# Kernel tuning notes

Hardware: AMD Instinct MI355X
Metric: run time of the kernel (lower is better)

The kernel has to match this reference:

```python
import jax, jax.numpy as jnp
import numpy as np

D = 2048
N_PASSES = 2
TOKENS = 16384


def _wht_matrix(d):
    # Sylvester construction of the (unnormalized) Walsh-Hadamard matrix.
    h = np.array([[1.0]], dtype=np.float32)
    while h.shape[0] < d:
        h = np.block([[h, h], [h, -h]])
    return jnp.asarray(h)


def setup_inputs() -> dict:
    key = jax.random.key(0)
    kx, ks = jax.random.split(key)
    x = jax.random.normal(kx, (TOKENS, D), dtype=jnp.float32)
    # random +/-1 sign arrays, one per pass (buffers in the torch module)
    signs = (2 * jax.random.randint(ks, (N_PASSES, D), 0, 2) - 1).astype(jnp.int32)
    wht_mat = _wht_matrix(D)
    return {"x": x, "signs": signs, "wht_mat": wht_mat}


def reference(x, signs, wht_mat):
    # Cascaded SRHT: (sign flip -> dense WHT matmul) x n_passes, scale fused at end.
    final_scale = jnp.asarray(1.0 / (D ** (N_PASSES / 2.0)), dtype=x.dtype)
    s = signs.astype(x.dtype)
    out = x
    for i in range(N_PASSES):
        out = out * s[i]          # [tokens, d] broadcast sign flip
        out = out @ wht_mat       # [tokens, d] x [d, d]
    return out * final_scale
```

## Files before the change

### kernel.cpp

```cpp
#include <hip/hip_runtime.h>

#define DIM 2048

typedef unsigned int uint2v __attribute__((ext_vector_type(2)));

__device__ __forceinline__ float4 sign_flip(float4 v, uint4 s) {
  float4 r;
  r.x = __uint_as_float(__float_as_uint(v.x) ^ (s.x & 0x80000000u));
  r.y = __uint_as_float(__float_as_uint(v.y) ^ (s.y & 0x80000000u));
  r.z = __uint_as_float(__float_as_uint(v.z) ^ (s.z & 0x80000000u));
  r.w = __uint_as_float(__float_as_uint(v.w) ^ (s.w & 0x80000000u));
  return r;
}

#define BFLY(a, b) { float _t = (a); (a) = _t + (b); (b) = _t - (b); }

__device__ __forceinline__ void bf4_pair(float4 &a, float4 &b) {
  BFLY(a.x, b.x); BFLY(a.y, b.y); BFLY(a.z, b.z); BFLY(a.w, b.w);
}

__device__ __forceinline__ void bf_comps(float4 &a) {
  BFLY(a.x, a.y); BFLY(a.z, a.w);
  BFLY(a.x, a.z); BFLY(a.y, a.w);
}

__device__ __forceinline__ void bf_oct(float4 v[8]) {
  bf4_pair(v[0], v[1]); bf4_pair(v[2], v[3]);
  bf4_pair(v[4], v[5]); bf4_pair(v[6], v[7]);
  bf4_pair(v[0], v[2]); bf4_pair(v[1], v[3]);
  bf4_pair(v[4], v[6]); bf4_pair(v[5], v[7]);
  bf4_pair(v[0], v[4]); bf4_pair(v[1], v[5]);
  bf4_pair(v[2], v[6]); bf4_pair(v[3], v[7]);
}

__device__ __forceinline__ void bf_oct12(float4 v[8]) {
  bf4_pair(v[0], v[1]); bf4_pair(v[2], v[3]);
  bf4_pair(v[4], v[5]); bf4_pair(v[6], v[7]);
  bf4_pair(v[0], v[2]); bf4_pair(v[1], v[3]);
  bf4_pair(v[4], v[6]); bf4_pair(v[5], v[7]);
}

template <int CTRL>
__device__ __forceinline__ float dpp_mov(float x) {
  return __int_as_float(
      __builtin_amdgcn_mov_dpp(__float_as_int(x), CTRL, 0xF, 0xF, true));
}

template <int CTRL>
__device__ __forceinline__ void dpp_stage(float4 v[8], float sgn) {
  #pragma unroll
  for (int i = 0; i < 8; ++i) {
    float px = dpp_mov<CTRL>(v[i].x);
    float py = dpp_mov<CTRL>(v[i].y);
    float pz = dpp_mov<CTRL>(v[i].z);
    float pw = dpp_mov<CTRL>(v[i].w);
    v[i].x = fmaf(sgn, v[i].x, px);
    v[i].y = fmaf(sgn, v[i].y, py);
    v[i].z = fmaf(sgn, v[i].z, pz);
    v[i].w = fmaf(sgn, v[i].w, pw);
  }
}

__device__ __forceinline__ float pl16_bfly(float x, float sgn) {
  uint2v r = __builtin_amdgcn_permlane16_swap(
      __float_as_uint(x), __float_as_uint(x), false, false);
  return fmaf(sgn, __uint_as_float(r[1]), __uint_as_float(r[0]));
}

__device__ __forceinline__ void pl16_stage(float4 v[8], float sgn) {
  #pragma unroll
  for (int i = 0; i < 8; ++i) {
    v[i].x = pl16_bfly(v[i].x, sgn);
    v[i].y = pl16_bfly(v[i].y, sgn);
    v[i].z = pl16_bfly(v[i].z, sgn);
    v[i].w = pl16_bfly(v[i].w, sgn);
  }
}

__device__ __forceinline__ float pl32_bfly(float x, float sgn) {
  uint2v r = __builtin_amdgcn_permlane32_swap(
      __float_as_uint(x), __float_as_uint(x), false, false);
  return fmaf(sgn, __uint_as_float(r[1]), __uint_as_float(r[0]));
}

__device__ __forceinline__ void pl32_stage(float4 v[8], float sgn) {
  #pragma unroll
  for (int i = 0; i < 8; ++i) {
    v[i].x = pl32_bfly(v[i].x, sgn);
    v[i].y = pl32_bfly(v[i].y, sgn);
    v[i].z = pl32_bfly(v[i].z, sgn);
    v[i].w = pl32_bfly(v[i].w, sgn);
  }
}

__device__ __forceinline__ void lds_fence() {
  asm volatile("s_waitcnt lgkmcnt(0)" ::: "memory");
}

__device__ __forceinline__ void xchg(float4* __restrict__ W, float4 v[8],
                                     int lane) {
  const int m  = (lane >> 2) & 3;
  const int ls = lane & ~12;
  #pragma unroll
  for (int half = 0; half < 2; ++half) {
    const int cs = half * 4;
    #pragma unroll
    for (int c2 = 0; c2 < 4; ++c2)
      W[c2 * 64 + (lane ^ ((c2 & 1) << 2))] = v[cs + c2];
    lds_fence();
    #pragma unroll
    for (int c2 = 0; c2 < 4; ++c2)
      v[cs + c2] = W[m * 64 + ((ls | (c2 << 2)) ^ ((m & 1) << 2))];
    lds_fence();
  }
}

__global__ __launch_bounds__(256) void srht2_kernel(
    const float* __restrict__ x, const int* __restrict__ signs,
    float* __restrict__ out, int nrows) {
  __shared__ __align__(16) float4 lds[4][256];
  const int lane = threadIdx.x & 63;
  const int wv   = threadIdx.x >> 6;
  const int row  = blockIdx.x * 4 + wv;
  if (row >= nrows) return;

  float4* __restrict__ W = lds[wv];

  const float sgn1  = (lane & 1)  ? -1.0f : 1.0f;
  const float sgn2  = (lane & 2)  ? -1.0f : 1.0f;
  const float sgn16 = (lane & 16) ? -1.0f : 1.0f;
  const float sgn32 = (lane & 32) ? -1.0f : 1.0f;

  const float4* __restrict__ xr = (const float4*)(x + (size_t)row * DIM);
  const uint4*  __restrict__ s0 = (const uint4*)signs;
  const uint4*  __restrict__ s1 = (const uint4*)(signs + DIM);

  float4 v[8];
  #pragma unroll
  for (int c = 0; c < 8; ++c) v[c] = xr[c * 64 + lane];

  #pragma unroll
  for (int c = 0; c < 8; ++c) v[c] = sign_flip(v[c], s0[c * 64 + lane]);
  #pragma unroll
  for (int c = 0; c < 8; ++c) bf_comps(v[c]);
  dpp_stage<0xB1>(v, sgn1);
  dpp_stage<0x4E>(v, sgn2);
  pl16_stage(v, sgn16);
  pl32_stage(v, sgn32);
  bf_oct(v);

  xchg(W, v, lane);
  bf_oct12(v);

  const int sb = (lane & 3) | ((lane >> 4) << 4) | (((lane >> 2) & 3) << 6);
  #pragma unroll
  for (int c = 0; c < 8; ++c)
    v[c] = sign_flip(v[c], s1[sb + ((c & 3) << 2) + ((c >> 2) << 8)]);
  #pragma unroll
  for (int c = 0; c < 8; ++c) bf_comps(v[c]);
  dpp_stage<0xB1>(v, sgn1);
  dpp_stage<0x4E>(v, sgn2);
  pl16_stage(v, sgn16);
  pl32_stage(v, sgn32);
  bf_oct(v);

  xchg(W, v, lane);
  bf_oct12(v);

  const float sc = 1.0f / 2048.0f;
  float4* __restrict__ orow = (float4*)(out + (size_t)row * DIM);
  #pragma unroll
  for (int c = 0; c < 8; ++c) {
    float4 t = v[c];
    t.x *= sc; t.y *= sc; t.z *= sc; t.w *= sc;
    orow[c * 64 + lane] = t;
  }
}

extern "C" void kernel_launch(void* const* d_in, const int* in_sizes, int n_in,
                              void* d_out, int out_size, void* d_ws, size_t ws_size,
                              hipStream_t stream) {
  const float* x     = (const float*)d_in[0];
  const int*   signs = (const int*)d_in[1];
  float*       out   = (float*)d_out;
  const int nrows   = in_sizes[0] / DIM;
  const int nblocks = nrows / 4;
  hipLaunchKernelGGL(srht2_kernel, dim3(nblocks), dim3(256), 0, stream,
                     x, signs, out, nrows);
}
```

Measured before the change: 241.8 us.

## Process multiple rows per wave with register prefetch and bit-packed signs

Each wave now handles four consecutive rows, prefetching the next row into registers while the current row's Hadamard butterflies run. The sign vectors are loaded once per wave and packed into two 32-bit bitmasks, so they are not reloaded per row. The LDS exchange uses two buffers per wave, which halves the number of fence pairs. This is meant to hide global load latency and cut redundant sign traffic, but it raises register pressure and reduces the number of blocks to a quarter, which lowers parallelism.

```diff
diff --git a/kernel.cpp b/kernel.cpp
--- a/kernel.cpp
+++ b/kernel.cpp
@@ -1,17 +1,9 @@
 #include <hip/hip_runtime.h>
 
 #define DIM 2048
+#define KROWS 4
 
 typedef unsigned int uint2v __attribute__((ext_vector_type(2)));
-
-__device__ __forceinline__ float4 sign_flip(float4 v, uint4 s) {
-  float4 r;
-  r.x = __uint_as_float(__float_as_uint(v.x) ^ (s.x & 0x80000000u));
-  r.y = __uint_as_float(__float_as_uint(v.y) ^ (s.y & 0x80000000u));
-  r.z = __uint_as_float(__float_as_uint(v.z) ^ (s.z & 0x80000000u));
-  r.w = __uint_as_float(__float_as_uint(v.w) ^ (s.w & 0x80000000u));
-  return r;
-}
 
 #define BFLY(a, b) { float _t = (a); (a) = _t + (b); (b) = _t - (b); }
 
@@ -97,83 +89,115 @@
   asm volatile("s_waitcnt lgkmcnt(0)" ::: "memory");
 }
 
-__device__ __forceinline__ void xchg(float4* __restrict__ W, float4 v[8],
-                                     int lane) {
+__device__ __forceinline__ void sflip4(float4 &a, unsigned p, int base) {
+  a.x = __uint_as_float(__float_as_uint(a.x) ^ ((p << (31 - (base + 0))) & 0x80000000u));
+  a.y = __uint_as_float(__float_as_uint(a.y) ^ ((p << (31 - (base + 1))) & 0x80000000u));
+  a.z = __uint_as_float(__float_as_uint(a.z) ^ ((p << (31 - (base + 2))) & 0x80000000u));
+  a.w = __uint_as_float(__float_as_uint(a.w) ^ ((p << (31 - (base + 3))) & 0x80000000u));
+}
+
+__device__ __forceinline__ void xchg(float4* __restrict__ W0,
+                                     float4* __restrict__ W1,
+                                     float4 v[8], int lane) {
   const int m  = (lane >> 2) & 3;
   const int ls = lane & ~12;
   #pragma unroll
-  for (int half = 0; half < 2; ++half) {
-    const int cs = half * 4;
-    #pragma unroll
-    for (int c2 = 0; c2 < 4; ++c2)
-      W[c2 * 64 + (lane ^ ((c2 & 1) << 2))] = v[cs + c2];
-    lds_fence();
-    #pragma unroll
-    for (int c2 = 0; c2 < 4; ++c2)
-      v[cs + c2] = W[m * 64 + ((ls | (c2 << 2)) ^ ((m & 1) << 2))];
-    lds_fence();
-  }
+  for (int c2 = 0; c2 < 4; ++c2)
+    W0[c2 * 64 + (lane ^ ((c2 & 1) << 2))] = v[c2];
+  #pragma unroll
+  for (int c2 = 0; c2 < 4; ++c2)
+    W1[c2 * 64 + (lane ^ ((c2 & 1) << 2))] = v[4 + c2];
+  lds_fence();
+  #pragma unroll
+  for (int c2 = 0; c2 < 4; ++c2)
+    v[c2] = W0[m * 64 + ((ls | (c2 << 2)) ^ ((m & 1) << 2))];
+  #pragma unroll
+  for (int c2 = 0; c2 < 4; ++c2)
+    v[4 + c2] = W1[m * 64 + ((ls | (c2 << 2)) ^ ((m & 1) << 2))];
+  lds_fence();
 }
 
 __global__ __launch_bounds__(256) void srht2_kernel(
     const float* __restrict__ x, const int* __restrict__ signs,
     float* __restrict__ out, int nrows) {
-  __shared__ __align__(16) float4 lds[4][256];
+  __shared__ __align__(16) float4 lds[8][256];
   const int lane = threadIdx.x & 63;
   const int wv   = threadIdx.x >> 6;
-  const int row  = blockIdx.x * 4 + wv;
-  if (row >= nrows) return;
-
-  float4* __restrict__ W = lds[wv];
+  const int row0 = (blockIdx.x * 4 + wv) * KROWS;
+  if (row0 >= nrows) return;
+
+  float4* __restrict__ W0 = lds[wv * 2];
+  float4* __restrict__ W1 = lds[wv * 2 + 1];
 
   const float sgn1  = (lane & 1)  ? -1.0f : 1.0f;
   const float sgn2  = (lane & 2)  ? -1.0f : 1.0f;
   const float sgn16 = (lane & 16) ? -1.0f : 1.0f;
   const float sgn32 = (lane & 32) ? -1.0f : 1.0f;
 
-  const float4* __restrict__ xr = (const float4*)(x + (size_t)row * DIM);
-  const uint4*  __restrict__ s0 = (const uint4*)signs;
-  const uint4*  __restrict__ s1 = (const uint4*)(signs + DIM);
-
-  float4 v[8];
+  const uint4* __restrict__ s0 = (const uint4*)signs;
+  const uint4* __restrict__ s1 = (const uint4*)(signs + DIM);
+
+  unsigned ps0 = 0, ps1 = 0;
+  const int sb = (lane & 3) | ((lane >> 4) << 4) | (((lane >> 2) & 3) << 6);
+  #pragma unroll
+  for (int c = 0; c < 8; ++c) {
+    uint4 s = s0[c * 64 + lane];
+    ps0 |= (s.x >> 31) << (4 * c)     | (s.y >> 31) << (4 * c + 1)
+        |  (s.z >> 31) << (4 * c + 2) | (s.w >> 31) << (4 * c + 3);
+    uint4 t = s1[sb + ((c & 3) << 2) + ((c >> 2) << 8)];
+    ps1 |= (t.x >> 31) << (4 * c)     | (t.y >> 31) << (4 * c + 1)
+        |  (t.z >> 31) << (4 * c + 2) | (t.w >> 31) << (4 * c + 3);
+  }
+
+  const float4* __restrict__ xr   = (const float4*)(x + (size_t)row0 * DIM);
+  float4*       __restrict__ orow = (float4*)(out + (size_t)row0 * DIM);
+
+  float4 v[8], p[8];
   #pragma unroll
   for (int c = 0; c < 8; ++c) v[c] = xr[c * 64 + lane];
 
-  #pragma unroll
-  for (int c = 0; c < 8; ++c) v[c] = sign_flip(v[c], s0[c * 64 + lane]);
-  #pragma unroll
-  for (int c = 0; c < 8; ++c) bf_comps(v[c]);
-  dpp_stage<0xB1>(v, sgn1);
-  dpp_stage<0x4E>(v, sgn2);
-  pl16_stage(v, sgn16);
-  pl32_stage(v, sgn32);
-  bf_oct(v);
-
-  xchg(W, v, lane);
-  bf_oct12(v);
-
-  const int sb = (lane & 3) | ((lane >> 4) << 4) | (((lane >> 2) & 3) << 6);
-  #pragma unroll
-  for (int c = 0; c < 8; ++c)
-    v[c] = sign_flip(v[c], s1[sb + ((c & 3) << 2) + ((c >> 2) << 8)]);
-  #pragma unroll
-  for (int c = 0; c < 8; ++c) bf_comps(v[c]);
-  dpp_stage<0xB1>(v, sgn1);
-  dpp_stage<0x4E>(v, sgn2);
-  pl16_stage(v, sgn16);
-  pl32_stage(v, sgn32);
-  bf_oct(v);
-
-  xchg(W, v, lane);
-  bf_oct12(v);
-
-  const float sc = 1.0f / 2048.0f;
-  float4* __restrict__ orow = (float4*)(out + (size_t)row * DIM);
-  #pragma unroll
-  for (int c = 0; c < 8; ++c) {
-    float4 t = v[c];
-    t.x *= sc; t.y *= sc; t.z *= sc; t.w *= sc;
-    orow[c * 64 + lane] = t;
+  #pragma unroll 1
+  for (int k = 0; k < KROWS; ++k) {
+    if (k + 1 < KROWS) {
+      const float4* __restrict__ xrn = xr + (DIM / 4);
+      #pragma unroll
+      for (int c = 0; c < 8; ++c) p[c] = xrn[c * 64 + lane];
+    }
+
+    #pragma unroll
+    for (int c = 0; c < 8; ++c) { sflip4(v[c], ps0, 4 * c); bf_comps(v[c]); }
+    dpp_stage<0xB1>(v, sgn1);
+    dpp_stage<0x4E>(v, sgn2);
+    pl16_stage(v, sgn16);
+    pl32_stage(v, sgn32);
+    bf_oct(v);
+    xchg(W0, W1, v, lane);
+    bf_oct12(v);
+
+    #pragma unroll
+    for (int c = 0; c < 8; ++c) { sflip4(v[c], ps1, 4 * c); bf_comps(v[c]); }
+    dpp_stage<0xB1>(v, sgn1);
+    dpp_stage<0x4E>(v, sgn2);
+    pl16_stage(v, sgn16);
+    pl32_stage(v, sgn32);
+    bf_oct(v);
+    xchg(W0, W1, v, lane);
+    bf_oct12(v);
+
+    const float sc = 1.0f / 2048.0f;
+    #pragma unroll
+    for (int c = 0; c < 8; ++c) {
+      float4 t = v[c];
+      t.x *= sc; t.y *= sc; t.z *= sc; t.w *= sc;
+      orow[c * 64 + lane] = t;
+    }
+
+    if (k + 1 < KROWS) {
+      #pragma unroll
+      for (int c = 0; c < 8; ++c) v[c] = p[c];
+      xr   += DIM / 4;
+      orow += DIM / 4;
+    }
   }
 }
 
@@ -184,7 +208,7 @@
   const int*   signs = (const int*)d_in[1];
   float*       out   = (float*)d_out;
   const int nrows   = in_sizes[0] / DIM;
-  const int nblocks = nrows / 4;
+  const int nblocks = nrows / (4 * KROWS);
   hipLaunchKernelGGL(srht2_kernel, dim3(nblocks), dim3(256), 0, stream,
                      x, signs, out, nrows);
 }
```

Result: slower. 247.5 us (+2.4%).
